# Optimization experiments

Measured on AMD Instinct MI355X. Metric: run time of the kernel, lower is better.

The kernel has to match this reference:

```python
import jax, jax.numpy as jnp
import numpy as np

N = 10           # node count hardcoded in original module
FEAT_IN = 3      # position(2) + orientation(1)
FEAT_OUT = 16    # 'simple' mode
FEAT_CC = 2 * FEAT_OUT
B = 16384
NEG_SLOPE = 0.2


def _pair_index():
    # Faithful pair ordering: for node i, row 0 is the self-pair (i,i),
    # rows 1..N-1 are j != i in ascending order.
    idx = np.empty((N, N), dtype=np.int32)
    for i in range(N):
        idx[i, 0] = i
        idx[i, 1:] = [j for j in range(N) if j != i]
    return jnp.asarray(idx)


def setup_inputs() -> dict:
    key = jax.random.key(0)
    ks = jax.random.split(key, 12)
    s = 0.1
    return {
        "position": jax.random.normal(ks[0], (B, N, 2), dtype=jnp.float32),
        "orientation": jax.random.normal(ks[1], (B, N, 1), dtype=jnp.float32),
        # preliminary_transform: Linear(3 -> 16)
        "Wp": jax.random.normal(ks[2], (FEAT_IN, FEAT_OUT), dtype=jnp.float32) * s,
        "bp": jax.random.normal(ks[3], (FEAT_OUT,), dtype=jnp.float32) * s,
        # connectivity_net: Linear(32->32), LReLU, Linear(32->8), LReLU, Linear(8->2)
        "W1": jax.random.normal(ks[4], (FEAT_CC, 32), dtype=jnp.float32) * s,
        "b1": jax.random.normal(ks[5], (32,), dtype=jnp.float32) * s,
        "W2": jax.random.normal(ks[6], (32, 8), dtype=jnp.float32) * s,
        "b2": jax.random.normal(ks[7], (8,), dtype=jnp.float32) * s,
        "W3": jax.random.normal(ks[8], (8, 2), dtype=jnp.float32) * s,
        "b3": jax.random.normal(ks[9], (2,), dtype=jnp.float32) * s,
    }


def reference(position, orientation, Wp, bp, W1, b1, W2, b2, W3, b3):
    lrelu = lambda x: jnp.where(x >= 0, x, NEG_SLOPE * x)
    # [B, N, 3] -> [B, N, 16]
    feat = jnp.concatenate([position, orientation], axis=2) @ Wp + bp
    idx = _pair_index()                                   # [N, N]
    vj = feat[:, idx]                                     # [B, N, N, 16] gathered partners
    vi = jnp.broadcast_to(feat[:, :, None, :], vj.shape)  # [B, N, N, 16] source node
    pair = jnp.concatenate([vi, vj], axis=-1)             # [B, N, N, 32]
    h = lrelu(pair @ W1 + b1)
    h = lrelu(h @ W2 + b2)
    big_edge = h @ W3 + b3                                # [B, N, N, 2]
    adjacency = jnp.argmax(big_edge, axis=3)              # [B, N, N]
    return big_edge, adjacency
```

## Files before the change

### kernel.cpp

```cpp
#include <hip/hip_runtime.h>


constexpr int N_NODES = 10;
constexpr int G = 8;
constexpr int NODES = G * N_NODES;
constexpr int GSTRIDE = 68;
constexpr int EDGES = G * N_NODES * N_NODES;
constexpr float NEG = 0.2f;

__global__ __launch_bounds__(256, 4) void gpn_kernel(
    const float* __restrict__ pos,
    const float* __restrict__ ori,
    const float* __restrict__ Wp,
    const float* __restrict__ bp,
    const float* __restrict__ W1,
    const float* __restrict__ b1,
    const float* __restrict__ W2,
    const float* __restrict__ b2,
    const float* __restrict__ W3,
    const float* __restrict__ b3,
    float* __restrict__ out,
    int B)
{
    __shared__ float sW1[32 * 32];
    __shared__ float sWp[3 * 16];
    __shared__ float sbp[16];
    __shared__ float sb1[32];
    __shared__ float sM[3 * 64];
    __shared__ float sc[64];
    __shared__ float sx[NODES * 3];
    __shared__ float sg[NODES * GSTRIDE];

    const int t = threadIdx.x;
    const int bBase = blockIdx.x * G;

    for (int idx = t; idx < 32 * 32; idx += 256) sW1[idx] = W1[idx];
    if (t < 48)       sWp[t]      = Wp[t];
    else if (t < 64)  sbp[t - 48] = bp[t - 48];
    else if (t < 96)  sb1[t - 64] = b1[t - 64];

    if (t < G * N_NODES * 2) {
        int bl = t / 20, r = t % 20;
        int n = r >> 1, d = r & 1;
        sx[(bl * N_NODES + n) * 3 + d] = pos[bBase * (N_NODES * 2) + t];
    } else if (t < G * N_NODES * 2 + G * N_NODES) {
        int u = t - G * N_NODES * 2;
        sx[u * 3 + 2] = ori[bBase * N_NODES + u];
    }
    __syncthreads();

    if (t < 192) {
        int d = t >> 6, k = t & 63;
        int kk = (k < 32) ? k : (k - 32);
        int fo = (k < 32) ? 0 : 16;
        float acc = 0.f;
#pragma unroll
        for (int f = 0; f < 16; ++f)
            acc = fmaf(sWp[d * 16 + f], sW1[(fo + f) * 32 + kk], acc);
        sM[d * 64 + k] = acc;
    } else {
        int k = t - 192;
        int kk = (k < 32) ? k : (k - 32);
        int fo = (k < 32) ? 0 : 16;
        float acc = 0.f;
#pragma unroll
        for (int f = 0; f < 16; ++f)
            acc = fmaf(sbp[f], sW1[(fo + f) * 32 + kk], acc);
        if (k < 32) acc += sb1[k];
        sc[k] = acc;
    }
    __syncthreads();

    {
        int k = t & 63;
        int ng = t >> 6;
        float m0 = sM[k], m1 = sM[64 + k], m2 = sM[128 + k];
        float ck = sc[k];
        for (int n = ng; n < NODES; n += 4) {
            float g = fmaf(sx[n * 3 + 0], m0,
                      fmaf(sx[n * 3 + 1], m1,
                      fmaf(sx[n * 3 + 2], m2, ck)));
            sg[n * GSTRIDE + k] = g;
        }
    }
    __syncthreads();

    const float4* sg4 = (const float4*)sg;
    const size_t adjOff = (size_t)B * (N_NODES * N_NODES) * 2;

    for (int e = t; e < EDGES; e += 256) {
        int bl = e / 100, rem = e % 100;
        int i = rem / 10, c = rem % 10;
        int j = (c == 0) ? i : (((c - 1) < i) ? (c - 1) : c);
        int ni = bl * N_NODES + i;
        int nj = bl * N_NODES + j;

        float h1[32];
#pragma unroll
        for (int q = 0; q < 8; ++q) {
            float4 a = sg4[ni * (GSTRIDE / 4) + q];
            float4 b = sg4[nj * (GSTRIDE / 4) + 8 + q];
            float s0 = a.x + b.x, s1 = a.y + b.y, s2 = a.z + b.z, s3 = a.w + b.w;
            h1[4 * q + 0] = fmaxf(s0, NEG * s0);
            h1[4 * q + 1] = fmaxf(s1, NEG * s1);
            h1[4 * q + 2] = fmaxf(s2, NEG * s2);
            h1[4 * q + 3] = fmaxf(s3, NEG * s3);
        }

        float acc[8] = {0.f, 0.f, 0.f, 0.f, 0.f, 0.f, 0.f, 0.f};
#pragma unroll
        for (int k = 0; k < 32; ++k) {
            float h = h1[k];
#pragma unroll
            for (int m = 0; m < 8; ++m)
                acc[m] = fmaf(h, W2[k * 8 + m], acc[m]);
        }

        float e0 = 0.f, e1 = 0.f;
#pragma unroll
        for (int m = 0; m < 8; ++m) {
            float h2 = acc[m] + b2[m];
            h2 = fmaxf(h2, NEG * h2);
            e0 = fmaf(h2, W3[m * 2 + 0], e0);
            e1 = fmaf(h2, W3[m * 2 + 1], e1);
        }
        e0 += b3[0];
        e1 += b3[1];

        int E = bBase * (N_NODES * N_NODES) + e;
        ((float2*)out)[E] = make_float2(e0, e1);
        out[adjOff + E] = (e1 > e0) ? 1.0f : 0.0f;
    }
}

extern "C" void kernel_launch(void* const* d_in, const int* in_sizes, int n_in,
                              void* d_out, int out_size, void* d_ws, size_t ws_size,
                              hipStream_t stream) {
    const float* pos = (const float*)d_in[0];
    const float* ori = (const float*)d_in[1];
    const float* Wp  = (const float*)d_in[2];
    const float* bp  = (const float*)d_in[3];
    const float* W1  = (const float*)d_in[4];
    const float* b1  = (const float*)d_in[5];
    const float* W2  = (const float*)d_in[6];
    const float* b2  = (const float*)d_in[7];
    const float* W3  = (const float*)d_in[8];
    const float* b3  = (const float*)d_in[9];
    float* out = (float*)d_out;

    const int B = in_sizes[0] / (N_NODES * 2);
    const int nBlocks = B / G;

    gpn_kernel<<<nBlocks, 256, 0, stream>>>(pos, ori, Wp, bp, W1, b1, W2, b2,
                                            W3, b3, out, B);
}
```

Measured before the change: 112.9 us.

## Pack MLP math into float2 vector FMAs and alias shared weight buffers

```diff
diff --git a/kernel.cpp b/kernel.cpp
--- a/kernel.cpp
+++ b/kernel.cpp
@@ -1,14 +1,17 @@
 #include <hip/hip_runtime.h>
 
+
+typedef float v2f __attribute__((ext_vector_type(2)));
+typedef float v4f __attribute__((ext_vector_type(4)));
 
 constexpr int N_NODES = 10;
 constexpr int G = 8;
 constexpr int NODES = G * N_NODES;
 constexpr int GSTRIDE = 68;
-constexpr int EDGES = G * N_NODES * N_NODES;
+constexpr int EDGES = G * 100;
 constexpr float NEG = 0.2f;
 
-__global__ __launch_bounds__(256, 4) void gpn_kernel(
+__global__ __launch_bounds__(256, 6) void gpn_kernel(
     const float* __restrict__ pos,
     const float* __restrict__ ori,
     const float* __restrict__ Wp,
@@ -22,51 +25,50 @@
     float* __restrict__ out,
     int B)
 {
-    __shared__ float sW1[32 * 32];
-    __shared__ float sWp[3 * 16];
-    __shared__ float sbp[16];
-    __shared__ float sb1[32];
+    __shared__ union SU {
+        struct { float W1[1024]; float Wp[48]; float bp[16]; float b1[32]; } w;
+        float g[NODES * GSTRIDE];
+    } sU;
     __shared__ float sM[3 * 64];
     __shared__ float sc[64];
     __shared__ float sx[NODES * 3];
-    __shared__ float sg[NODES * GSTRIDE];
 
     const int t = threadIdx.x;
     const int bBase = blockIdx.x * G;
 
-    for (int idx = t; idx < 32 * 32; idx += 256) sW1[idx] = W1[idx];
-    if (t < 48)       sWp[t]      = Wp[t];
-    else if (t < 64)  sbp[t - 48] = bp[t - 48];
-    else if (t < 96)  sb1[t - 64] = b1[t - 64];
+    for (int idx = t; idx < 1024; idx += 256) sU.w.W1[idx] = W1[idx];
+    if (t < 48)       sU.w.Wp[t]      = Wp[t];
+    else if (t < 64)  sU.w.bp[t - 48] = bp[t - 48];
+    else if (t < 96)  sU.w.b1[t - 64] = b1[t - 64];
 
-    if (t < G * N_NODES * 2) {
-        int bl = t / 20, r = t % 20;
-        int n = r >> 1, d = r & 1;
-        sx[(bl * N_NODES + n) * 3 + d] = pos[bBase * (N_NODES * 2) + t];
-    } else if (t < G * N_NODES * 2 + G * N_NODES) {
-        int u = t - G * N_NODES * 2;
+    if (t < NODES * 2) {
+        int u = t;
+        int n = u >> 1, d = u & 1;
+        sx[n * 3 + d] = pos[bBase * (N_NODES * 2) + u];
+    } else if (t < NODES * 2 + NODES) {
+        int u = t - NODES * 2;
         sx[u * 3 + 2] = ori[bBase * N_NODES + u];
     }
     __syncthreads();
 
     if (t < 192) {
         int d = t >> 6, k = t & 63;
-        int kk = (k < 32) ? k : (k - 32);
+        int kk = k & 31;
         int fo = (k < 32) ? 0 : 16;
         float acc = 0.f;
 #pragma unroll
         for (int f = 0; f < 16; ++f)
-            acc = fmaf(sWp[d * 16 + f], sW1[(fo + f) * 32 + kk], acc);
+            acc = fmaf(sU.w.Wp[d * 16 + f], sU.w.W1[(fo + f) * 32 + kk], acc);
         sM[d * 64 + k] = acc;
-    } else {
+    } else if (t < 256) {
         int k = t - 192;
-        int kk = (k < 32) ? k : (k - 32);
+        int kk = k & 31;
         int fo = (k < 32) ? 0 : 16;
         float acc = 0.f;
 #pragma unroll
         for (int f = 0; f < 16; ++f)
-            acc = fmaf(sbp[f], sW1[(fo + f) * 32 + kk], acc);
-        if (k < 32) acc += sb1[k];
+            acc = fmaf(sU.w.bp[f], sU.w.W1[(fo + f) * 32 + kk], acc);
+        if (k < 32) acc += sU.w.b1[k];
         sc[k] = acc;
     }
     __syncthreads();
@@ -80,56 +82,75 @@
             float g = fmaf(sx[n * 3 + 0], m0,
                       fmaf(sx[n * 3 + 1], m1,
                       fmaf(sx[n * 3 + 2], m2, ck)));
-            sg[n * GSTRIDE + k] = g;
+            sU.g[n * GSTRIDE + k] = g;
         }
     }
     __syncthreads();
 
-    const float4* sg4 = (const float4*)sg;
-    const size_t adjOff = (size_t)B * (N_NODES * N_NODES) * 2;
+    const v4f* g4 = (const v4f*)sU.g;
+    const v2f* w2p = (const v2f*)W2;
+    const v2f* w3p = (const v2f*)W3;
+    const v2f* b2p = (const v2f*)b2;
+    const v2f* b3p = (const v2f*)b3;
+    const size_t adjOff = (size_t)B * 200;
 
     for (int e = t; e < EDGES; e += 256) {
-        int bl = e / 100, rem = e % 100;
-        int i = rem / 10, c = rem % 10;
+        int bl = e / 100, rem = e - bl * 100;
+        int i = rem / 10, c = rem - i * 10;
         int j = (c == 0) ? i : (((c - 1) < i) ? (c - 1) : c);
-        int ni = bl * N_NODES + i;
-        int nj = bl * N_NODES + j;
+        const int ra = (bl * N_NODES + i) * (GSTRIDE / 4);
+        const int rb = (bl * N_NODES + j) * (GSTRIDE / 4) + 8;
 
-        float h1[32];
+        v2f h[16];
 #pragma unroll
         for (int q = 0; q < 8; ++q) {
-            float4 a = sg4[ni * (GSTRIDE / 4) + q];
-            float4 b = sg4[nj * (GSTRIDE / 4) + 8 + q];
-            float s0 = a.x + b.x, s1 = a.y + b.y, s2 = a.z + b.z, s3 = a.w + b.w;
-            h1[4 * q + 0] = fmaxf(s0, NEG * s0);
-            h1[4 * q + 1] = fmaxf(s1, NEG * s1);
-            h1[4 * q + 2] = fmaxf(s2, NEG * s2);
-            h1[4 * q + 3] = fmaxf(s3, NEG * s3);
+            v4f a = g4[ra + q];
+            v4f b = g4[rb + q];
+            v4f s = a + b;
+            v4f hh = __builtin_elementwise_max(s, s * NEG);
+            h[2 * q + 0] = hh.xy;
+            h[2 * q + 1] = hh.zw;
         }
 
-        float acc[8] = {0.f, 0.f, 0.f, 0.f, 0.f, 0.f, 0.f, 0.f};
+        v2f a0 = b2p[0], a1 = b2p[1], a2 = b2p[2], a3 = b2p[3];
 #pragma unroll
-        for (int k = 0; k < 32; ++k) {
-            float h = h1[k];
-#pragma unroll
-            for (int m = 0; m < 8; ++m)
-                acc[m] = fmaf(h, W2[k * 8 + m], acc[m]);
+        for (int k2 = 0; k2 < 16; ++k2) {
+            v2f hp = h[k2];
+            v2f hx = {hp.x, hp.x};
+            v2f hy = {hp.y, hp.y};
+            const int k0 = 2 * k2, k1 = 2 * k2 + 1;
+            a0 = __builtin_elementwise_fma(hx, w2p[4 * k0 + 0], a0);
+            a1 = __builtin_elementwise_fma(hx, w2p[4 * k0 + 1], a1);
+            a2 = __builtin_elementwise_fma(hx, w2p[4 * k0 + 2], a2);
+            a3 = __builtin_elementwise_fma(hx, w2p[4 * k0 + 3], a3);
+            a0 = __builtin_elementwise_fma(hy, w2p[4 * k1 + 0], a0);
+            a1 = __builtin_elementwise_fma(hy, w2p[4 * k1 + 1], a1);
+            a2 = __builtin_elementwise_fma(hy, w2p[4 * k1 + 2], a2);
+            a3 = __builtin_elementwise_fma(hy, w2p[4 * k1 + 3], a3);
         }
 
-        float e0 = 0.f, e1 = 0.f;
-#pragma unroll
-        for (int m = 0; m < 8; ++m) {
-            float h2 = acc[m] + b2[m];
-            h2 = fmaxf(h2, NEG * h2);
-            e0 = fmaf(h2, W3[m * 2 + 0], e0);
-            e1 = fmaf(h2, W3[m * 2 + 1], e1);
-        }
-        e0 += b3[0];
-        e1 += b3[1];
+        v2f h20 = __builtin_elementwise_max(a0, a0 * NEG);
+        v2f h21 = __builtin_elementwise_max(a1, a1 * NEG);
+        v2f h22 = __builtin_elementwise_max(a2, a2 * NEG);
+        v2f h23 = __builtin_elementwise_max(a3, a3 * NEG);
 
-        int E = bBase * (N_NODES * N_NODES) + e;
-        ((float2*)out)[E] = make_float2(e0, e1);
-        out[adjOff + E] = (e1 > e0) ? 1.0f : 0.0f;
+        v2f ev = b3p[0];
+        v2f s0 = {h20.x, h20.x}, s1 = {h20.y, h20.y};
+        ev = __builtin_elementwise_fma(s0, w3p[0], ev);
+        ev = __builtin_elementwise_fma(s1, w3p[1], ev);
+        v2f s2 = {h21.x, h21.x}, s3 = {h21.y, h21.y};
+        ev = __builtin_elementwise_fma(s2, w3p[2], ev);
+        ev = __builtin_elementwise_fma(s3, w3p[3], ev);
+        v2f s4 = {h22.x, h22.x}, s5 = {h22.y, h22.y};
+        ev = __builtin_elementwise_fma(s4, w3p[4], ev);
+        ev = __builtin_elementwise_fma(s5, w3p[5], ev);
+        v2f s6 = {h23.x, h23.x}, s7 = {h23.y, h23.y};
+        ev = __builtin_elementwise_fma(s6, w3p[6], ev);
+        ev = __builtin_elementwise_fma(s7, w3p[7], ev);
+
+        const int E = bBase * 100 + e;
+        ((v2f*)out)[E] = ev;
+        out[adjOff + E] = (ev.y > ev.x) ? 1.0f : 0.0f;
     }
 }
 
```

New measurement: 109.0 us. -3.4%, faster.

## Assign one thread per source node computing all ten edges with packed-FMA math

Applied to the files above, without the earlier changes.

```diff
diff --git a/kernel.cpp b/kernel.cpp
--- a/kernel.cpp
+++ b/kernel.cpp
@@ -1,11 +1,11 @@
 #include <hip/hip_runtime.h>
 
 
-constexpr int N_NODES = 10;
-constexpr int G = 8;
-constexpr int NODES = G * N_NODES;
-constexpr int GSTRIDE = 68;
-constexpr int EDGES = G * N_NODES * N_NODES;
+typedef float v2f __attribute__((ext_vector_type(2)));
+typedef float v4f __attribute__((ext_vector_type(4)));
+
+constexpr int G = 25;
+constexpr int GB_STRIDE = 36;
 constexpr float NEG = 0.2f;
 
 __global__ __launch_bounds__(256, 4) void gpn_kernel(
@@ -22,114 +22,135 @@
     float* __restrict__ out,
     int B)
 {
-    __shared__ float sW1[32 * 32];
-    __shared__ float sWp[3 * 16];
-    __shared__ float sbp[16];
-    __shared__ float sb1[32];
     __shared__ float sM[3 * 64];
     __shared__ float sc[64];
-    __shared__ float sx[NODES * 3];
-    __shared__ float sg[NODES * GSTRIDE];
+    __shared__ float sgb[G * 10 * GB_STRIDE];
 
     const int t = threadIdx.x;
     const int bBase = blockIdx.x * G;
-
-    for (int idx = t; idx < 32 * 32; idx += 256) sW1[idx] = W1[idx];
-    if (t < 48)       sWp[t]      = Wp[t];
-    else if (t < 64)  sbp[t - 48] = bp[t - 48];
-    else if (t < 96)  sb1[t - 64] = b1[t - 64];
-
-    if (t < G * N_NODES * 2) {
-        int bl = t / 20, r = t % 20;
-        int n = r >> 1, d = r & 1;
-        sx[(bl * N_NODES + n) * 3 + d] = pos[bBase * (N_NODES * 2) + t];
-    } else if (t < G * N_NODES * 2 + G * N_NODES) {
-        int u = t - G * N_NODES * 2;
-        sx[u * 3 + 2] = ori[bBase * N_NODES + u];
-    }
-    __syncthreads();
-
-    if (t < 192) {
-        int d = t >> 6, k = t & 63;
-        int kk = (k < 32) ? k : (k - 32);
-        int fo = (k < 32) ? 0 : 16;
-        float acc = 0.f;
-#pragma unroll
-        for (int f = 0; f < 16; ++f)
-            acc = fmaf(sWp[d * 16 + f], sW1[(fo + f) * 32 + kk], acc);
-        sM[d * 64 + k] = acc;
-    } else {
-        int k = t - 192;
-        int kk = (k < 32) ? k : (k - 32);
-        int fo = (k < 32) ? 0 : 16;
-        float acc = 0.f;
-#pragma unroll
-        for (int f = 0; f < 16; ++f)
-            acc = fmaf(sbp[f], sW1[(fo + f) * 32 + kk], acc);
-        if (k < 32) acc += sb1[k];
-        sc[k] = acc;
-    }
-    __syncthreads();
+    const int remG = B - bBase;
+    const int nNodes = ((remG < G) ? remG : G) * 10;
 
     {
-        int k = t & 63;
-        int ng = t >> 6;
-        float m0 = sM[k], m1 = sM[64 + k], m2 = sM[128 + k];
-        float ck = sc[k];
-        for (int n = ng; n < NODES; n += 4) {
-            float g = fmaf(sx[n * 3 + 0], m0,
-                      fmaf(sx[n * 3 + 1], m1,
-                      fmaf(sx[n * 3 + 2], m2, ck)));
-            sg[n * GSTRIDE + k] = g;
+        if (t < 192) {
+            const int d = t >> 6, k = t & 63;
+            const int kk = k & 31;
+            const int fo = (k < 32) ? 0 : 16;
+            float acc = 0.f;
+#pragma unroll
+            for (int f = 0; f < 16; ++f)
+                acc = fmaf(Wp[d * 16 + f], W1[(fo + f) * 32 + kk], acc);
+            sM[d * 64 + k] = acc;
+        } else {
+            const int k = t - 192;
+            const int kk = k & 31;
+            const int fo = (k < 32) ? 0 : 16;
+            float acc = 0.f;
+#pragma unroll
+            for (int f = 0; f < 16; ++f)
+                acc = fmaf(bp[f], W1[(fo + f) * 32 + kk], acc);
+            if (k < 32) acc += b1[k];
+            sc[k] = acc;
         }
     }
     __syncthreads();
 
-    const float4* sg4 = (const float4*)sg;
-    const size_t adjOff = (size_t)B * (N_NODES * N_NODES) * 2;
+    v4f ga[8];
+    const int g = t / 10;
+    const int i = t - g * 10;
+    if (t < nNodes) {
+        const int node = bBase * 10 + t;
+        const v2f p = ((const v2f*)pos)[node];
+        const float o = ori[node];
+        const v4f* m4 = (const v4f*)sM;
+        const v4f* c4 = (const v4f*)sc;
+        v4f* dst = (v4f*)&sgb[t * GB_STRIDE];
+#pragma unroll
+        for (int q = 0; q < 16; ++q) {
+            v4f gg = c4[q];
+            gg += p.x * m4[q];
+            gg += p.y * m4[16 + q];
+            gg += o   * m4[32 + q];
+            if (q < 8) ga[q] = gg;
+            else       dst[q - 8] = gg;
+        }
+    }
+    __syncthreads();
 
-    for (int e = t; e < EDGES; e += 256) {
-        int bl = e / 100, rem = e % 100;
-        int i = rem / 10, c = rem % 10;
-        int j = (c == 0) ? i : (((c - 1) < i) ? (c - 1) : c);
-        int ni = bl * N_NODES + i;
-        int nj = bl * N_NODES + j;
+    if (t < nNodes) {
+        const v2f* w2p = (const v2f*)W2;
+        const v2f* w3p = (const v2f*)W3;
+        const v2f bb2_0 = ((const v2f*)b2)[0];
+        const v2f bb2_1 = ((const v2f*)b2)[1];
+        const v2f bb2_2 = ((const v2f*)b2)[2];
+        const v2f bb2_3 = ((const v2f*)b2)[3];
+        const v2f bb3   = ((const v2f*)b3)[0];
 
-        float h1[32];
+        float evb[20];
+        float adj[10];
+
 #pragma unroll
-        for (int q = 0; q < 8; ++q) {
-            float4 a = sg4[ni * (GSTRIDE / 4) + q];
-            float4 b = sg4[nj * (GSTRIDE / 4) + 8 + q];
-            float s0 = a.x + b.x, s1 = a.y + b.y, s2 = a.z + b.z, s3 = a.w + b.w;
-            h1[4 * q + 0] = fmaxf(s0, NEG * s0);
-            h1[4 * q + 1] = fmaxf(s1, NEG * s1);
-            h1[4 * q + 2] = fmaxf(s2, NEG * s2);
-            h1[4 * q + 3] = fmaxf(s3, NEG * s3);
+        for (int c = 0; c < 10; ++c) {
+            const int j = (c == 0) ? i : (((c - 1) < i) ? (c - 1) : c);
+            const v4f* src = (const v4f*)&sgb[(g * 10 + j) * GB_STRIDE];
+
+            v2f a0 = bb2_0, a1 = bb2_1, a2 = bb2_2, a3 = bb2_3;
+#pragma unroll
+            for (int q = 0; q < 8; ++q) {
+                const v4f s = ga[q] + src[q];
+                const v4f h = __builtin_elementwise_max(s, s * NEG);
+                const int k0 = 4 * q;
+                a0 += h.x * w2p[4 * (k0 + 0) + 0];
+                a1 += h.x * w2p[4 * (k0 + 0) + 1];
+                a2 += h.x * w2p[4 * (k0 + 0) + 2];
+                a3 += h.x * w2p[4 * (k0 + 0) + 3];
+                a0 += h.y * w2p[4 * (k0 + 1) + 0];
+                a1 += h.y * w2p[4 * (k0 + 1) + 1];
+                a2 += h.y * w2p[4 * (k0 + 1) + 2];
+                a3 += h.y * w2p[4 * (k0 + 1) + 3];
+                a0 += h.z * w2p[4 * (k0 + 2) + 0];
+                a1 += h.z * w2p[4 * (k0 + 2) + 1];
+                a2 += h.z * w2p[4 * (k0 + 2) + 2];
+                a3 += h.z * w2p[4 * (k0 + 2) + 3];
+                a0 += h.w * w2p[4 * (k0 + 3) + 0];
+                a1 += h.w * w2p[4 * (k0 + 3) + 1];
+                a2 += h.w * w2p[4 * (k0 + 3) + 2];
+                a3 += h.w * w2p[4 * (k0 + 3) + 3];
+            }
+
+            const v2f h20 = __builtin_elementwise_max(a0, a0 * NEG);
+            const v2f h21 = __builtin_elementwise_max(a1, a1 * NEG);
+            const v2f h22 = __builtin_elementwise_max(a2, a2 * NEG);
+            const v2f h23 = __builtin_elementwise_max(a3, a3 * NEG);
+
+            v2f ev = bb3;
+            ev += h20.x * w3p[0];
+            ev += h20.y * w3p[1];
+            ev += h21.x * w3p[2];
+            ev += h21.y * w3p[3];
+            ev += h22.x * w3p[4];
+            ev += h22.y * w3p[5];
+            ev += h23.x * w3p[6];
+            ev += h23.y * w3p[7];
+
+            evb[2 * c]     = ev.x;
+            evb[2 * c + 1] = ev.y;
+            adj[c] = (ev.y > ev.x) ? 1.0f : 0.0f;
         }
 
-        float acc[8] = {0.f, 0.f, 0.f, 0.f, 0.f, 0.f, 0.f, 0.f};
+        const int eBase = (bBase * 10 + t) * 10;
+        v4f* bo = (v4f*)(out + (size_t)eBase * 2);
 #pragma unroll
-        for (int k = 0; k < 32; ++k) {
-            float h = h1[k];
+        for (int q = 0; q < 5; ++q) {
+            v4f vv = {evb[4 * q], evb[4 * q + 1], evb[4 * q + 2], evb[4 * q + 3]};
+            bo[q] = vv;
+        }
+        v2f* ao = (v2f*)(out + (size_t)B * 200 + eBase);
 #pragma unroll
-            for (int m = 0; m < 8; ++m)
-                acc[m] = fmaf(h, W2[k * 8 + m], acc[m]);
+        for (int q = 0; q < 5; ++q) {
+            v2f vv = {adj[2 * q], adj[2 * q + 1]};
+            ao[q] = vv;
         }
-
-        float e0 = 0.f, e1 = 0.f;
-#pragma unroll
-        for (int m = 0; m < 8; ++m) {
-            float h2 = acc[m] + b2[m];
-            h2 = fmaxf(h2, NEG * h2);
-            e0 = fmaf(h2, W3[m * 2 + 0], e0);
-            e1 = fmaf(h2, W3[m * 2 + 1], e1);
-        }
-        e0 += b3[0];
-        e1 += b3[1];
-
-        int E = bBase * (N_NODES * N_NODES) + e;
-        ((float2*)out)[E] = make_float2(e0, e1);
-        out[adjOff + E] = (e1 > e0) ? 1.0f : 0.0f;
     }
 }
 
@@ -148,8 +169,8 @@
     const float* b3  = (const float*)d_in[9];
     float* out = (float*)d_out;
 
-    const int B = in_sizes[0] / (N_NODES * 2);
-    const int nBlocks = B / G;
+    const int B = in_sizes[0] / 20;
+    const int nBlocks = (B + G - 1) / G;
 
     gpn_kernel<<<nBlocks, 256, 0, stream>>>(pos, ori, Wp, bp, W1, b1, W2, b2,
                                             W3, b3, out, B);
```

Result: faster. 104.0 us (-7.9%).
